# Kernel optimization log

Measured on AMD Instinct MI355X. Metric: run time of the kernel, lower is better.

Reference implementation:

```python
import jax, jax.numpy as jnp
import numpy as np

B, NA, T, NV, D = 24, 50, 10, 196, 512


def setup_inputs() -> dict:
    key = jax.random.key(0)
    k1, k2 = jax.random.split(key)
    return {
        "audio_feats": jax.random.normal(k1, (B, NA, D), dtype=jnp.float32),
        "visual_feats": jax.random.normal(k2, (B, T, NV, D), dtype=jnp.float32),
        "temperature": jnp.float32(2.5),
        "scale_factor": jnp.float32(2.5),
        "threshold": jnp.float32(-2.5),
    }


def _l2norm(x):
    # F.normalize(dim=-1): x / max(||x||, 1e-12)
    n = jnp.sqrt(jnp.sum(x * x, axis=-1, keepdims=True))
    return x / jnp.maximum(n, 1e-12)


def reference(audio_feats, visual_feats, temperature, scale_factor, threshold):
    b = audio_feats.shape[0]
    a = _l2norm(audio_feats)          # (B,Na,D)
    v = _l2norm(visual_feats)         # (B,T,Nv,D)
    # all-pairs token similarities: (B,B,Na,T,Nv)
    sims = jnp.einsum('xad,ytvd->xyatv', a, v) / temperature

    # aggregate_temporal_similarities
    th = jax.nn.sigmoid(threshold)
    max_vis = jnp.max(sims, axis=-1)            # (B,B,Na,T)
    raw_diff = max_vis - th
    sel = jax.nn.relu(raw_diff) * scale_factor  # selection strength
    weighted_sum = jnp.sum(max_vis * sel, axis=-1)   # over T
    weights_sum = jnp.sum(sel, axis=-1)
    token_sims = weighted_sum / jnp.maximum(weights_sum, 1e-6)
    clip_sims = jnp.mean(token_sims, axis=-1)   # (B,B)
    fraction_selected = jnp.mean((raw_diff > 0).astype(jnp.float32))

    # InfoNCE
    idx = jnp.arange(b)
    losses_a2v = -jax.nn.log_softmax(clip_sims, axis=1)[idx, idx]
    losses_v2a = -jax.nn.log_softmax(clip_sims.T, axis=1)[idx, idx]
    contrastive_loss = jnp.mean(losses_a2v + losses_v2a) / 2

    # regularization
    neg = jnp.clip(sims, -20.0, 0.0)
    l_nonneg = jnp.mean(neg * neg)
    temp_low = jnp.maximum(-jnp.log(temperature), 0.0) ** 2   # log(1)=0
    temp_high = jnp.maximum(jnp.log(temperature) - jnp.log(4.0), 0.0) ** 2
    l_cal = temp_low + temp_high
    l_threshold = jnp.maximum(th - 0.9, 0.0) ** 2 + jnp.maximum(0.1 - th, 0.0) ** 2
    l_scale = jnp.maximum(scale_factor - 20.0, 0.0) ** 2 + jnp.maximum(1.0 - scale_factor, 0.0) ** 2
    reg_loss = 0.15 * l_nonneg + 2.0 * l_cal + 0.1 * l_threshold + 0.1 * l_scale

    # selection reward on positive pairs (diagonal)
    pos_diffs = raw_diff[idx, idx]                       # (B,Na,T)
    sel_ratio = (jnp.tanh(20.0 * pos_diffs) + 1.0) / 2.0
    selection_reward = -0.1 * jnp.log1p(jnp.mean(sel_ratio))

    total_loss = selection_reward + contrastive_loss + reg_loss
    return (total_loss, contrastive_loss, reg_loss, fraction_selected, selection_reward)
```

## Files before the change

### kernel.cpp

```cpp
#include <hip/hip_runtime.h>
#include <math.h>

#define B_   24
#define NA_  50
#define T_   10
#define NV_  196
#define D_   512
#define M_   1200
#define MPAD 1280
#define NVP  224
#define YT_  240
#define VROWS (YT_ * NVP)
#define ABLK 320

#define NT    16
#define BUFB  32768u
#define VBASE 16384u

typedef __bf16 bf16x8 __attribute__((ext_vector_type(8)));
typedef float  f32x4  __attribute__((ext_vector_type(4)));
typedef unsigned short ushort8 __attribute__((ext_vector_type(8)));

__device__ __forceinline__ unsigned short f2bf(float f) {
    unsigned u = __float_as_uint(f);
    u += 0x7FFF + ((u >> 16) & 1);
    return (unsigned short)(u >> 16);
}

__device__ __forceinline__ void gload16(const void* g, void* l) {
    __builtin_amdgcn_global_load_lds(
        (const __attribute__((address_space(1))) unsigned int*)g,
        (__attribute__((address_space(3))) unsigned int*)l, 16, 0, 0);
}

__global__ void normconv_kernel(const float* __restrict__ a,
                                const float* __restrict__ vf,
                                const float* __restrict__ tempPtr,
                                unsigned short* __restrict__ Abf,
                                unsigned short* __restrict__ Vbf,
                                float* __restrict__ accs) {
    if (blockIdx.x == 0 && threadIdx.x < 4) accs[threadIdx.x] = 0.0f;
    int w = threadIdx.x >> 6, lane = threadIdx.x & 63;
    int bid = blockIdx.x;
    const float* src = nullptr;
    ushort8* dst;
    float tscale = 1.0f;
    if (bid < ABLK) {
        int row = bid * 4 + w;
        dst = (ushort8*)(Abf + (size_t)row * D_ + lane * 8);
        if (row < M_) { src = a + (size_t)row * D_ + lane * 8; tscale = tempPtr[0]; }
    } else {
        int row = (bid - ABLK) * 4 + w;
        dst = (ushort8*)(Vbf + (size_t)row * D_ + lane * 8);
        int yt = row / NVP, vv = row - yt * NVP;
        if (vv < NV_) src = vf + ((size_t)yt * NV_ + vv) * D_ + lane * 8;
    }
    if (src) {
        float4 u = *(const float4*)src;
        float4 v = *(const float4*)(src + 4);
        float s = u.x*u.x + u.y*u.y + u.z*u.z + u.w*u.w
                + v.x*v.x + v.y*v.y + v.z*v.z + v.w*v.w;
        #pragma unroll
        for (int off = 32; off; off >>= 1) s += __shfl_xor(s, off, 64);
        float sc = 1.0f / (fmaxf(sqrtf(s), 1e-12f) * tscale);
        ushort8 o;
        o[0]=f2bf(u.x*sc); o[1]=f2bf(u.y*sc); o[2]=f2bf(u.z*sc); o[3]=f2bf(u.w*sc);
        o[4]=f2bf(v.x*sc); o[5]=f2bf(v.y*sc); o[6]=f2bf(v.z*sc); o[7]=f2bf(v.w*sc);
        *dst = o;
    } else {
        ushort8 z = (ushort8)0;
        *dst = z;
    }
}

__global__ __launch_bounds__(512, 1) void simred_kernel(
    const unsigned short* __restrict__ Abf, const unsigned short* __restrict__ Vbf,
    float* __restrict__ maxvis, float* __restrict__ accNonneg)
{
    __shared__ __align__(16) unsigned char lds[2 * BUFB];
    float* maxredp = (float*)(lds + 30720);
    float* redbufp = (float*)(lds + BUFB + 30720);

    const int tid  = threadIdx.x;
    const int lane = tid & 63;
    const int w    = tid >> 6;
    const int lrow = lane >> 2;
    const int lcol = lane & 3;
    const int q    = lane >> 4;
    const int m16  = lane & 15;
    const int wr   = w & 3;
    const int wc   = w >> 2;

    const int lin = blockIdx.y * gridDim.x + blockIdx.x;
    const int swz = (lin & 7) * 150 + (lin >> 3);
    const int bx  = swz % 5;
    const int yt  = swz / 5;
    const int rowA0 = bx * 256;
    const size_t vRow0 = (size_t)yt * NVP;

    const int scol = lcol ^ ((lrow >> 1) & 3);
    const unsigned short* gp[4];
    unsigned loff[4];
    #pragma unroll
    for (int k = 0; k < 4; ++k) {
        int u = w + 8 * k;
        if (u < 16)      gp[k] = Abf + ((size_t)(rowA0 + u * 16 + lrow)) * D_ + scol * 8;
        else if (u < 30) gp[k] = Vbf + (vRow0 + (size_t)((u - 16) * 16 + lrow)) * D_ + scol * 8;
        else             gp[k] = Abf + (size_t)lane * 8;
        loff[k] = (unsigned)u * 1024u;
    }

    const unsigned rsw = (unsigned)((m16 >> 1) & 3) * 16u;
    unsigned aoff[4], boff[7];
    #pragma unroll
    for (int i = 0; i < 4; ++i)
        aoff[i] = (unsigned)(wr * 64 + i * 16 + m16) * 64u + (((unsigned)q * 16u) ^ rsw);
    #pragma unroll
    for (int j = 0; j < 7; ++j)
        boff[j] = VBASE + (unsigned)(wc * 112 + j * 16 + m16) * 64u + (((unsigned)q * 16u) ^ rsw);

    f32x4 acc[4][7];
    #pragma unroll
    for (int i = 0; i < 4; ++i)
        #pragma unroll
        for (int j = 0; j < 7; ++j) acc[i][j] = (f32x4)0.0f;

    #pragma unroll
    for (int k = 0; k < 4; ++k) gload16(gp[k], (void*)(lds + loff[k]));
    #pragma unroll
    for (int k = 0; k < 4; ++k) gload16(gp[k] + 32, (void*)(lds + BUFB + loff[k]));
    asm volatile("s_waitcnt vmcnt(4)\ns_barrier" ::: "memory");

    #pragma unroll 2
    for (int t = 0; t < NT; ++t) {
        const unsigned char* buf = lds + (unsigned)(t & 1) * BUFB;
        bf16x8 af[4], bv[7];
        #pragma unroll
        for (int i = 0; i < 4; ++i) af[i] = *(const bf16x8*)(buf + aoff[i]);
        #pragma unroll
        for (int j = 0; j < 7; ++j) bv[j] = *(const bf16x8*)(buf + boff[j]);
        asm volatile("s_waitcnt lgkmcnt(0)\ns_barrier" ::: "memory");
        __builtin_amdgcn_sched_barrier(0);
        if (t < NT - 2) {
            const int kc2 = (t + 2) * 32;
            #pragma unroll
            for (int k = 0; k < 4; ++k)
                gload16(gp[k] + kc2, (void*)(lds + (unsigned)(t & 1) * BUFB + loff[k]));
        }
        __builtin_amdgcn_sched_barrier(0);
        __builtin_amdgcn_s_setprio(1);
        #pragma unroll
        for (int i = 0; i < 4; ++i)
            #pragma unroll
            for (int j = 0; j < 7; ++j)
                acc[i][j] = __builtin_amdgcn_mfma_f32_16x16x32_bf16(af[i], bv[j], acc[i][j], 0, 0, 0);
        __builtin_amdgcn_s_setprio(0);
        if (t < NT - 2)       asm volatile("s_waitcnt vmcnt(4)\ns_barrier" ::: "memory");
        else if (t == NT - 2) asm volatile("s_waitcnt vmcnt(0)\ns_barrier" ::: "memory");
    }

    float cs = 0.0f;
    #pragma unroll
    for (int i = 0; i < 4; ++i)
        #pragma unroll
        for (int j = 0; j < 7; ++j)
            #pragma unroll
            for (int r = 0; r < 4; ++r) {
                float v = acc[i][j][r];
                float cv = fminf(fmaxf(v, -20.0f), 0.0f);
                cs += cv * cv;
            }
    #pragma unroll
    for (int off = 32; off; off >>= 1) cs += __shfl_xor(cs, off, 64);
    if (lane == 0) redbufp[w] = cs;

    bool colv[7];
    #pragma unroll
    for (int j = 0; j < 7; ++j) colv[j] = (wc * 112 + j * 16 + m16) < NV_;
    #pragma unroll
    for (int i = 0; i < 4; ++i) {
        float mx[4] = {-3e38f, -3e38f, -3e38f, -3e38f};
        #pragma unroll
        for (int j = 0; j < 7; ++j)
            #pragma unroll
            for (int r = 0; r < 4; ++r)
                mx[r] = fmaxf(mx[r], colv[j] ? acc[i][j][r] : -3e38f);
        #pragma unroll
        for (int r = 0; r < 4; ++r) {
            float mm = mx[r];
            #pragma unroll
            for (int off = 1; off <= 8; off <<= 1) mm = fmaxf(mm, __shfl_xor(mm, off, 64));
            if (m16 == 0) maxredp[wc * 256 + wr * 64 + i * 16 + q * 4 + r] = mm;
        }
    }
    __syncthreads();
    if (tid == 0) atomicAdd(accNonneg, redbufp[0] + redbufp[1] + redbufp[2] + redbufp[3]
                                     + redbufp[4] + redbufp[5] + redbufp[6] + redbufp[7]);
    if (tid < 256) {
        float mm = fmaxf(maxredp[tid], maxredp[256 + tid]);
        int R = rowA0 + tid;
        if (R < M_) {
            int x = R / NA_, a = R - x * NA_;
            int y = yt / T_, t = yt - y * T_;
            maxvis[(((size_t)x * B_ + y) * NA_ + a) * T_ + t] = mm;
        }
    }
}

__global__ void aggfin_kernel(const float* __restrict__ maxvis,
                              const float* __restrict__ thrPtr,
                              const float* __restrict__ scalePtr,
                              const float* __restrict__ tempPtr,
                              float* __restrict__ clipSims,
                              float* __restrict__ accs,
                              float* __restrict__ out)
{
    int xy = blockIdx.x;
    int x = xy / B_, y = xy % B_;
    int a = threadIdx.x;
    float th    = 1.0f / (1.0f + expf(-thrPtr[0]));
    float scale = scalePtr[0];
    float token = 0.0f, cnt = 0.0f, selsum = 0.0f;
    if (a < NA_) {
        const float* p = maxvis + (((size_t)x * B_ + y) * NA_ + a) * T_;
        float ws = 0.0f, ss = 0.0f;
        #pragma unroll
        for (int t = 0; t < T_; ++t) {
            float mv  = p[t];
            float rd  = mv - th;
            float sel = fmaxf(rd, 0.0f) * scale;
            ws += mv * sel;
            ss += sel;
            if (rd > 0.0f) cnt += 1.0f;
            if (x == y) selsum += 0.5f * (tanhf(20.0f * rd) + 1.0f);
        }
        token = ws / fmaxf(ss, 1e-6f);
    }
    #pragma unroll
    for (int off = 32; off; off >>= 1) {
        token  += __shfl_xor(token,  off, 64);
        cnt    += __shfl_xor(cnt,    off, 64);
        selsum += __shfl_xor(selsum, off, 64);
    }
    if (threadIdx.x == 0) {
        clipSims[x * B_ + y] = token / (float)NA_;
        atomicAdd(&accs[1], cnt);
        if (x == y) atomicAdd(&accs[2], selsum);
    }
    __threadfence();
    unsigned last = 0;
    if (threadIdx.x == 0) {
        unsigned v = atomicAdd((unsigned int*)(accs + 3), 1u);
        last = ((v % (unsigned)(B_ * B_)) == (unsigned)(B_ * B_ - 1));
    }
    last = __shfl((int)last, 0, 64);
    if (!last) return;
    __threadfence();

    __shared__ float cs[B_ * B_];
    int tid = threadIdx.x;
    for (int i = tid; i < B_ * B_; i += 64) cs[i] = clipSims[i];
    __syncthreads();
    float lsum = 0.0f;
    if (tid < B_) {
        int i = tid;
        float m = -1e30f;
        for (int j = 0; j < B_; ++j) m = fmaxf(m, cs[i * B_ + j]);
        float e = 0.0f;
        for (int j = 0; j < B_; ++j) e += expf(cs[i * B_ + j] - m);
        float la = m + logf(e) - cs[i * B_ + i];
        float m2 = -1e30f;
        for (int j = 0; j < B_; ++j) m2 = fmaxf(m2, cs[j * B_ + i]);
        float e2 = 0.0f;
        for (int j = 0; j < B_; ++j) e2 += expf(cs[j * B_ + i] - m2);
        float lv = m2 + logf(e2) - cs[i * B_ + i];
        lsum = la + lv;
    }
    #pragma unroll
    for (int off = 32; off; off >>= 1) lsum += __shfl_xor(lsum, off, 64);
    if (tid == 0) {
        float contrastive = lsum / (float)B_ * 0.5f;
        float temp = tempPtr[0], scl = scalePtr[0];
        float l_nonneg = accs[0] / 56448000.0f;
        float logt = logf(temp);
        float tl  = fmaxf(-logt, 0.0f);
        float thi = fmaxf(logt - logf(4.0f), 0.0f);
        float l_cal = tl * tl + thi * thi;
        float t1 = fmaxf(th - 0.9f, 0.0f), t2 = fmaxf(0.1f - th, 0.0f);
        float l_thr = t1 * t1 + t2 * t2;
        float s1 = fmaxf(scl - 20.0f, 0.0f), s2 = fmaxf(1.0f - scl, 0.0f);
        float l_scale = s1 * s1 + s2 * s2;
        float reg = 0.15f * l_nonneg + 2.0f * l_cal + 0.1f * l_thr + 0.1f * l_scale;
        float frac   = accs[1] / 288000.0f;
        float selrew = -0.1f * log1pf(accs[2] / 12000.0f);
        out[0] = selrew + contrastive + reg;
        out[1] = contrastive;
        out[2] = reg;
        out[3] = frac;
        out[4] = selrew;
    }
}

extern "C" void kernel_launch(void* const* d_in, const int* in_sizes, int n_in,
                              void* d_out, int out_size, void* d_ws, size_t ws_size,
                              hipStream_t stream) {
    const float* audio  = (const float*)d_in[0];
    const float* visual = (const float*)d_in[1];
    const float* temp   = (const float*)d_in[2];
    const float* scale  = (const float*)d_in[3];
    const float* thr    = (const float*)d_in[4];
    float* out = (float*)d_out;

    unsigned char* wsb = (unsigned char*)d_ws;
    unsigned short* Abf = (unsigned short*)wsb;
    unsigned short* Vbf = (unsigned short*)(wsb + 1310720);
    float* maxvis   = (float*)(wsb + 1310720 + 55050240);
    float* clipSims = (float*)(wsb + 1310720 + 55050240 + 1152000);
    float* accs     = clipSims + 576;

    normconv_kernel<<<ABLK + VROWS / 4, 256, 0, stream>>>(audio, visual, temp, Abf, Vbf, accs);

    dim3 grid(MPAD / 256, YT_);
    simred_kernel<<<grid, 512, 0, stream>>>(Abf, Vbf, maxvis, accs);

    aggfin_kernel<<<B_ * B_, 64, 0, stream>>>(maxvis, thr, scale, temp, clipSims, accs, out);
}
```

Baseline: 277.4 us.

## Double-buffer MFMA fragments in registers to overlap LDS reads with MFMAs

Unrolls the K loop by two and keeps two register sets of A/B fragments. The next tile's fragments are read from LDS while MFMAs run on the current set, which is meant to hide LDS read latency behind matrix math. In exchange, global-to-LDS staging now waits on vmcnt(0) at every half-step, so global loads get only one half-iteration of lead instead of two, and register pressure rises. It also recomputes the sigmoid threshold from the input for the threshold regularizer in the finalize step.

```diff
diff --git a/kernel.cpp b/kernel.cpp
--- a/kernel.cpp
+++ b/kernel.cpp
@@ -73,6 +73,21 @@
     }
 }
 
+#define RD_FRAGS(AF, BV, BASE)                                                  \
+    _Pragma("unroll") for (int i = 0; i < 4; ++i)                               \
+        AF[i] = *(const bf16x8*)((BASE) + aoff[i]);                             \
+    _Pragma("unroll") for (int j = 0; j < 7; ++j)                               \
+        BV[j] = *(const bf16x8*)((BASE) + boff[j]);
+
+#define MFMA_ALL(AF, BV)                                                        \
+    _Pragma("unroll") for (int i = 0; i < 4; ++i)                               \
+        _Pragma("unroll") for (int j = 0; j < 7; ++j)                           \
+            acc[i][j] = __builtin_amdgcn_mfma_f32_16x16x32_bf16(AF[i], BV[j], acc[i][j], 0, 0, 0);
+
+#define STAGE_T(T, BASEOFF)                                                     \
+    _Pragma("unroll") for (int k = 0; k < 4; ++k)                               \
+        gload16(gp[k] + (T) * 32, (void*)(lds + (BASEOFF) + loff[k]));
+
 __global__ __launch_bounds__(512, 1) void simred_kernel(
     const unsigned short* __restrict__ Abf, const unsigned short* __restrict__ Vbf,
     float* __restrict__ maxvis, float* __restrict__ accNonneg)
@@ -125,38 +140,28 @@
         #pragma unroll
         for (int j = 0; j < 7; ++j) acc[i][j] = (f32x4)0.0f;
 
-    #pragma unroll
-    for (int k = 0; k < 4; ++k) gload16(gp[k], (void*)(lds + loff[k]));
-    #pragma unroll
-    for (int k = 0; k < 4; ++k) gload16(gp[k] + 32, (void*)(lds + BUFB + loff[k]));
+    bf16x8 afA[4], bvA[7], afB[4], bvB[7];
+
+    STAGE_T(0, 0u)
+    STAGE_T(1, BUFB)
     asm volatile("s_waitcnt vmcnt(4)\ns_barrier" ::: "memory");
-
-    #pragma unroll 2
-    for (int t = 0; t < NT; ++t) {
-        const unsigned char* buf = lds + (unsigned)(t & 1) * BUFB;
-        bf16x8 af[4], bv[7];
-        #pragma unroll
-        for (int i = 0; i < 4; ++i) af[i] = *(const bf16x8*)(buf + aoff[i]);
-        #pragma unroll
-        for (int j = 0; j < 7; ++j) bv[j] = *(const bf16x8*)(buf + boff[j]);
-        asm volatile("s_waitcnt lgkmcnt(0)\ns_barrier" ::: "memory");
-        __builtin_amdgcn_sched_barrier(0);
-        if (t < NT - 2) {
-            const int kc2 = (t + 2) * 32;
-            #pragma unroll
-            for (int k = 0; k < 4; ++k)
-                gload16(gp[k] + kc2, (void*)(lds + (unsigned)(t & 1) * BUFB + loff[k]));
-        }
-        __builtin_amdgcn_sched_barrier(0);
+    RD_FRAGS(afA, bvA, lds)
+
+    #pragma unroll
+    for (int tp = 0; tp < 8; ++tp) {
+        const int t = 2 * tp;
+        asm volatile("s_waitcnt vmcnt(0) lgkmcnt(0)\ns_barrier" ::: "memory");
+        if (t + 2 < NT) { STAGE_T(t + 2, 0u) }
+        RD_FRAGS(afB, bvB, lds + BUFB)
         __builtin_amdgcn_s_setprio(1);
-        #pragma unroll
-        for (int i = 0; i < 4; ++i)
-            #pragma unroll
-            for (int j = 0; j < 7; ++j)
-                acc[i][j] = __builtin_amdgcn_mfma_f32_16x16x32_bf16(af[i], bv[j], acc[i][j], 0, 0, 0);
+        MFMA_ALL(afA, bvA)
         __builtin_amdgcn_s_setprio(0);
-        if (t < NT - 2)       asm volatile("s_waitcnt vmcnt(4)\ns_barrier" ::: "memory");
-        else if (t == NT - 2) asm volatile("s_waitcnt vmcnt(0)\ns_barrier" ::: "memory");
+        asm volatile("s_waitcnt vmcnt(0) lgkmcnt(0)\ns_barrier" ::: "memory");
+        if (t + 3 < NT) { STAGE_T(t + 3, BUFB) }
+        if (t + 2 < NT) { RD_FRAGS(afA, bvA, lds) }
+        __builtin_amdgcn_s_setprio(1);
+        MFMA_ALL(afB, bvB)
+        __builtin_amdgcn_s_setprio(0);
     }
 
     float cs = 0.0f;
@@ -281,12 +286,13 @@
     if (tid == 0) {
         float contrastive = lsum / (float)B_ * 0.5f;
         float temp = tempPtr[0], scl = scalePtr[0];
+        float th2 = 1.0f / (1.0f + expf(-thrPtr[0]));
         float l_nonneg = accs[0] / 56448000.0f;
         float logt = logf(temp);
         float tl  = fmaxf(-logt, 0.0f);
         float thi = fmaxf(logt - logf(4.0f), 0.0f);
         float l_cal = tl * tl + thi * thi;
-        float t1 = fmaxf(th - 0.9f, 0.0f), t2 = fmaxf(0.1f - th, 0.0f);
+        float t1 = fmaxf(th2 - 0.9f, 0.0f), t2 = fmaxf(0.1f - th2, 0.0f);
         float l_thr = t1 * t1 + t2 * t2;
         float s1 = fmaxf(scl - 20.0f, 0.0f), s2 = fmaxf(1.0f - scl, 0.0f);
         float l_scale = s1 * s1 + s2 * s2;
```

Result: faster. 266.8 us (-3.8%).
